# Kernel optimization log

Hardware: AMD Instinct MI355X
Metric: run time of the kernel (lower is better)

## Reference

```python
import jax, jax.numpy as jnp
import numpy as np

N_NODES = 100000
EMB_DIM = 64
HIDDEN = 8
OUT_DIM = 16
NUM_HEADS = 3
B = 1024
E_RAND = 3200000


def setup_inputs() -> dict:
    key = jax.random.key(0)
    ks = jax.random.split(key, 12)
    src = jax.random.randint(ks[0], (E_RAND,), 0, N_NODES, dtype=jnp.int32)
    dst = jax.random.randint(ks[1], (E_RAND,), 0, N_NODES, dtype=jnp.int32)
    loop = jnp.arange(N_NODES, dtype=jnp.int32)
    src = jnp.concatenate([src, loop])
    dst = jnp.concatenate([dst, loop])
    # multi-hot query indicator, ~50 items per query, guarantee >=1 item
    queries = (jax.random.uniform(ks[2], (B, N_NODES)) < 5e-4).astype(jnp.float32)
    queries = queries.at[:, 0].set(1.0)
    pos_items = jax.random.randint(ks[3], (B,), 0, N_NODES, dtype=jnp.int32)
    neg_items = jax.random.randint(ks[4], (B,), 0, N_NODES, dtype=jnp.int32)
    embedding = jax.random.normal(ks[5], (N_NODES, EMB_DIM), dtype=jnp.float32) * 0.1
    # GAT layer 1: NUM_HEADS heads, in=64 -> out=8 per head (concat)
    W1 = jax.random.normal(ks[6], (NUM_HEADS, EMB_DIM, HIDDEN), dtype=jnp.float32) * 0.1
    a1 = jax.random.normal(ks[7], (NUM_HEADS, 2 * HIDDEN), dtype=jnp.float32) * 0.1
    # GAT layer 2: 1 head, in=24 -> out=16
    W2 = jax.random.normal(ks[8], (NUM_HEADS * HIDDEN, OUT_DIM), dtype=jnp.float32) * 0.1
    a2 = jax.random.normal(ks[9], (2 * OUT_DIM,), dtype=jnp.float32) * 0.1
    return {"queries": queries, "pos_items": pos_items, "neg_items": neg_items,
            "embedding": embedding, "W1": W1, "a1": a1, "W2": W2, "a2": a2,
            "src": src, "dst": dst}


def gat_layer(h, W, a, src, dst, n_nodes):
    # h: [N, in], W: [H, in, o], a: [H, 2o]; returns [N, H, o]
    o = W.shape[-1]
    z = jnp.einsum('nd,hdo->nho', h, W)            # [N,H,o]
    zs, zd = z[src], z[dst]                         # [E,H,o]
    e = jax.nn.leaky_relu(
        jnp.einsum('eho,ho->eh', zs, a[:, :o]) +
        jnp.einsum('eho,ho->eh', zd, a[:, o:]), 0.01)  # [E,H]
    m = jax.ops.segment_max(e, dst, num_segments=n_nodes)       # [N,H]
    alpha = jnp.exp(e - m[dst])                                  # [E,H]
    denom = jax.ops.segment_sum(alpha, dst, num_segments=n_nodes)
    num = jax.ops.segment_sum(alpha[:, :, None] * zs, dst, num_segments=n_nodes)
    return num / denom[:, :, None]


def gat_forward(embedding, W1, a1, W2, a2, src, dst):
    n = embedding.shape[0]
    h1 = gat_layer(embedding, W1, a1, src, dst, n)       # [N,H,hid]
    h1 = jax.nn.elu(h1.reshape(n, -1))                   # [N,H*hid]
    h2 = gat_layer(h1, W2[None], a2[None], src, dst, n)  # [N,1,out]
    return h2[:, 0]                                      # [N,out]


def reference(queries, pos_items, neg_items, embedding, W1, a1, W2, a2, src, dst):
    item_embeds = gat_forward(embedding, W1, a1, W2, a2, src, dst)  # [N,16]
    item_cnt = jnp.sum(queries, axis=1)                              # [B]
    query_embeds = jnp.matmul(queries, item_embeds) / item_cnt[:, None]
    pos_embed = item_embeds[pos_items]
    neg_embed = item_embeds[neg_items]
    return (query_embeds, pos_embed, neg_embed)
```

## Files before the change

kernel.cpp:

```cpp
#include <hip/hip_runtime.h>

#define NH 3
#define HID 8
#define C1 24
#define C2 16
#define BSH 5
#define BNODES 32
#define NBMAX 3200
#define SCAP 1792
#define PCHUNK 16384
#define AZS 32

__global__ __launch_bounds__(256) void k_z1(
    const float* __restrict__ emb, const float* __restrict__ W1g,
    const float* __restrict__ a1g, float* __restrict__ az1,
    float4* __restrict__ f1d, int N) {
    __shared__ float sW[NH * 64 * HID];
    __shared__ float sa[NH * 2 * HID];
    for (int i = threadIdx.x; i < NH * 64 * HID; i += blockDim.x) sW[i] = W1g[i];
    for (int i = threadIdx.x; i < NH * 2 * HID; i += blockDim.x) sa[i] = a1g[i];
    __syncthreads();
    int n = blockIdx.x * blockDim.x + threadIdx.x;
    if (n >= N) return;
    float e[64];
    const float4* ep = (const float4*)(emb + (size_t)n * 64);
#pragma unroll
    for (int i = 0; i < 16; ++i) {
        float4 v = ep[i];
        e[4*i+0] = v.x; e[4*i+1] = v.y; e[4*i+2] = v.z; e[4*i+3] = v.w;
    }
    float z[C1];
#pragma unroll
    for (int c = 0; c < C1; ++c) z[c] = 0.f;
    for (int d = 0; d < 64; ++d) {
        float ed = e[d];
#pragma unroll
        for (int h = 0; h < NH; ++h) {
            const float4* wp = (const float4*)&sW[(h * 64 + d) * HID];
            float4 w0 = wp[0], w1 = wp[1];
            z[h*HID+0] += ed * w0.x; z[h*HID+1] += ed * w0.y;
            z[h*HID+2] += ed * w0.z; z[h*HID+3] += ed * w0.w;
            z[h*HID+4] += ed * w1.x; z[h*HID+5] += ed * w1.y;
            z[h*HID+6] += ed * w1.z; z[h*HID+7] += ed * w1.w;
        }
    }
    float fs[NH], fd[NH];
#pragma unroll
    for (int h = 0; h < NH; ++h) {
        float s = 0.f, dsum = 0.f;
#pragma unroll
        for (int o = 0; o < HID; ++o) {
            s    += z[h*HID+o] * sa[h*2*HID + o];
            dsum += z[h*HID+o] * sa[h*2*HID + HID + o];
        }
        fs[h] = s; fd[h] = dsum;
    }
    float4* zp = (float4*)(az1 + (size_t)n * AZS);
    zp[0] = make_float4(fs[0], fs[1], fs[2], 0.f);
#pragma unroll
    for (int i = 0; i < 6; ++i)
        zp[1 + i] = make_float4(z[4*i], z[4*i+1], z[4*i+2], z[4*i+3]);
    zp[7] = make_float4(0.f, 0.f, 0.f, 0.f);
    f1d[n] = make_float4(fd[0], fd[1], fd[2], 0.f);
}

__global__ void k_zero(int* __restrict__ p, int n) {
    int i = blockIdx.x * blockDim.x + threadIdx.x;
    if (i < n) p[i] = 0;
}

__global__ __launch_bounds__(256) void k_count(const int* __restrict__ dst,
                                               int* __restrict__ bcnt, int E, int NB) {
    __shared__ int lh[NBMAX];
    for (int i = threadIdx.x; i < NB; i += 256) lh[i] = 0;
    __syncthreads();
    int base = blockIdx.x * PCHUNK;
    int end = base + PCHUNK; if (end > E) end = E;
    for (int i = base + threadIdx.x; i < end; i += 256)
        atomicAdd(&lh[dst[i] >> BSH], 1);
    __syncthreads();
    for (int i = threadIdx.x; i < NB; i += 256)
        if (lh[i]) atomicAdd(&bcnt[i], lh[i]);
}

#define SCANK 13
__global__ __launch_bounds__(256) void k_bscan(const int* __restrict__ bcnt,
                                               int* __restrict__ boff,
                                               int* __restrict__ bcur,
                                               int* __restrict__ rowptr,
                                               int NB, int N, int E) {
    __shared__ int sd[256];
    int tid = threadIdx.x;
    int v[SCANK]; int tsum = 0;
#pragma unroll
    for (int i = 0; i < SCANK; ++i) {
        int g = tid * SCANK + i;
        v[i] = (g < NB) ? bcnt[g] : 0;
        tsum += v[i];
    }
    sd[tid] = tsum; __syncthreads();
    for (int off = 1; off < 256; off <<= 1) {
        int t = (tid >= off) ? sd[tid - off] : 0;
        __syncthreads();
        sd[tid] += t;
        __syncthreads();
    }
    int pref = sd[tid] - tsum;
#pragma unroll
    for (int i = 0; i < SCANK; ++i) {
        int g = tid * SCANK + i;
        if (g < NB) { boff[g] = pref; bcur[g] = pref; pref += v[i]; }
    }
    if (tid == 255) boff[NB] = pref;
    if (tid == 0) rowptr[N] = E;
}

__global__ __launch_bounds__(256) void k_part(const int* __restrict__ src,
                                              const int* __restrict__ dst,
                                              int* __restrict__ bcur,
                                              int* __restrict__ bedges, int E, int NB) {
    __shared__ int lh[NBMAX];
    __shared__ int lbase[NBMAX];
    for (int i = threadIdx.x; i < NB; i += 256) lh[i] = 0;
    __syncthreads();
    int base = blockIdx.x * PCHUNK;
    int end = base + PCHUNK; if (end > E) end = E;
    for (int i = base + threadIdx.x; i < end; i += 256)
        atomicAdd(&lh[dst[i] >> BSH], 1);
    __syncthreads();
    for (int i = threadIdx.x; i < NB; i += 256) {
        int c = lh[i];
        lbase[i] = c ? atomicAdd(&bcur[i], c) : 0;
        lh[i] = 0;
    }
    __syncthreads();
    for (int i = base + threadIdx.x; i < end; i += 256) {
        int d = dst[i];
        int b = d >> BSH;
        int p = lbase[b] + atomicAdd(&lh[b], 1);
        bedges[p] = src[i] | ((d & (BNODES - 1)) << 17);
    }
}

__global__ __launch_bounds__(256) void k_gat1(
    const int* __restrict__ boff, int* __restrict__ bedges,
    const float* __restrict__ az1, const float4* __restrict__ f1d,
    const float* __restrict__ W2g, const float* __restrict__ a2g,
    float* __restrict__ z2, float* __restrict__ f2s, float* __restrict__ f2d,
    int* __restrict__ rowptr, int N) {
    __shared__ int ssrc[SCAP];
    __shared__ int scnt[BNODES];
    __shared__ int sstart[BNODES + 1];
    __shared__ int scur[BNODES];
    __shared__ float sW2[C1 * C2];
    __shared__ float sa2[2 * C2];
    int tid = threadIdx.x;
    int b = blockIdx.x;
    int beg = boff[b], cnt = boff[b + 1] - beg;
    if (tid < BNODES) scnt[tid] = 0;
    for (int i = tid; i < C1 * C2; i += 256) sW2[i] = W2g[i];
    if (tid < 2 * C2) sa2[tid] = a2g[tid];
    __syncthreads();
    for (int i = tid; i < cnt; i += 256)
        atomicAdd(&scnt[bedges[beg + i] >> 17], 1);
    __syncthreads();
    if (tid < BNODES) {
        int v = scnt[tid];
        int x = v;
        for (int d = 1; d < BNODES; d <<= 1) {
            int t = __shfl_up(x, d, 64);
            if (tid >= d) x += t;
        }
        sstart[tid] = x - v;
        scur[tid] = x - v;
        if (tid == BNODES - 1) sstart[BNODES] = x;
    }
    __syncthreads();
    for (int i = tid; i < cnt; i += 256) {
        int pk = bedges[beg + i];
        int p = atomicAdd(&scur[pk >> 17], 1);
        ssrc[p] = pk & 0x1FFFF;
    }
    __syncthreads();
    for (int i = tid; i < cnt; i += 256) bedges[beg + i] = ssrc[i];
    int n0 = b << BSH;
    if (tid < BNODES) rowptr[n0 + tid] = beg + sstart[tid];
    int nl = tid >> 3, l8 = tid & 7;
    int n = n0 + nl;
    int s0 = sstart[nl], s1 = sstart[nl + 1];
    float4 fdv = (n < N) ? f1d[n] : make_float4(0.f, 0.f, 0.f, 0.f);
    float acc[C1];
#pragma unroll
    for (int c = 0; c < C1; ++c) acc[c] = 0.f;
    float den0 = 0.f, den1 = 0.f, den2 = 0.f;
    for (int i = s0 + l8; i < s1; i += 8) {
        int s = ssrc[i];
        const float4* zp = (const float4*)(az1 + ((size_t)s << 5));
        float4 q0 = zp[0], q1 = zp[1], q2 = zp[2], q3 = zp[3],
               q4 = zp[4], q5 = zp[5], q6 = zp[6];
        float e0 = q0.x + fdv.x, e1 = q0.y + fdv.y, e2 = q0.z + fdv.z;
        e0 = e0 > 0.f ? e0 : 0.01f * e0;
        e1 = e1 > 0.f ? e1 : 0.01f * e1;
        e2 = e2 > 0.f ? e2 : 0.01f * e2;
        float a0 = __expf(e0), a1 = __expf(e1), a2v = __expf(e2);
        den0 += a0; den1 += a1; den2 += a2v;
        acc[0]  += a0 * q1.x; acc[1]  += a0 * q1.y; acc[2]  += a0 * q1.z; acc[3]  += a0 * q1.w;
        acc[4]  += a0 * q2.x; acc[5]  += a0 * q2.y; acc[6]  += a0 * q2.z; acc[7]  += a0 * q2.w;
        acc[8]  += a1 * q3.x; acc[9]  += a1 * q3.y; acc[10] += a1 * q3.z; acc[11] += a1 * q3.w;
        acc[12] += a1 * q4.x; acc[13] += a1 * q4.y; acc[14] += a1 * q4.z; acc[15] += a1 * q4.w;
        acc[16] += a2v * q5.x; acc[17] += a2v * q5.y; acc[18] += a2v * q5.z; acc[19] += a2v * q5.w;
        acc[20] += a2v * q6.x; acc[21] += a2v * q6.y; acc[22] += a2v * q6.z; acc[23] += a2v * q6.w;
    }
#pragma unroll
    for (int c = 0; c < C1; ++c) {
        acc[c] += __shfl_xor(acc[c], 1, 64);
        acc[c] += __shfl_xor(acc[c], 2, 64);
        acc[c] += __shfl_xor(acc[c], 4, 64);
    }
    den0 += __shfl_xor(den0, 1, 64); den0 += __shfl_xor(den0, 2, 64); den0 += __shfl_xor(den0, 4, 64);
    den1 += __shfl_xor(den1, 1, 64); den1 += __shfl_xor(den1, 2, 64); den1 += __shfl_xor(den1, 4, 64);
    den2 += __shfl_xor(den2, 1, 64); den2 += __shfl_xor(den2, 2, 64); den2 += __shfl_xor(den2, 4, 64);
    if (l8 == 0 && n < N) {
        float h1v[C1];
        float inv0 = 1.f / den0, inv1 = 1.f / den1, inv2 = 1.f / den2;
#pragma unroll
        for (int o = 0; o < HID; ++o) {
            float v0 = acc[o] * inv0;
            float v1 = acc[HID + o] * inv1;
            float v2 = acc[2 * HID + o] * inv2;
            h1v[o]           = v0 > 0.f ? v0 : (__expf(v0) - 1.f);
            h1v[HID + o]     = v1 > 0.f ? v1 : (__expf(v1) - 1.f);
            h1v[2 * HID + o] = v2 > 0.f ? v2 : (__expf(v2) - 1.f);
        }
        float zz[C2];
#pragma unroll
        for (int k = 0; k < C2; ++k) zz[k] = 0.f;
        for (int c = 0; c < C1; ++c) {
            float hv = h1v[c];
#pragma unroll
            for (int k = 0; k < C2; ++k) zz[k] += hv * sW2[c * C2 + k];
        }
        float fs = 0.f, fdd = 0.f;
#pragma unroll
        for (int k = 0; k < C2; ++k) {
            fs  += zz[k] * sa2[k];
            fdd += zz[k] * sa2[C2 + k];
        }
        float4* zo = (float4*)(z2 + (size_t)n * C2);
#pragma unroll
        for (int i = 0; i < 4; ++i)
            zo[i] = make_float4(zz[4*i], zz[4*i+1], zz[4*i+2], zz[4*i+3]);
        f2s[n] = fs;
        f2d[n] = fdd;
    }
}

__global__ __launch_bounds__(256) void k_gat2(
    const int* __restrict__ rowptr, const int* __restrict__ csr,
    const float* __restrict__ z2, const float* __restrict__ f2s,
    const float* __restrict__ f2d, float* __restrict__ item, int N) {
    int t = blockIdx.x * blockDim.x + threadIdx.x;
    int n = t >> 3, l8 = t & 7;
    if (n >= N) return;
    int beg = rowptr[n], end = rowptr[n + 1];
    float fdv = f2d[n];
    float acc[C2];
#pragma unroll
    for (int k = 0; k < C2; ++k) acc[k] = 0.f;
    float den = 0.f;
    for (int i = beg + l8; i < end; i += 8) {
        int s = csr[i];
        float e = f2s[s] + fdv;
        e = e > 0.f ? e : 0.01f * e;
        float a = __expf(e);
        den += a;
        const float4* zp = (const float4*)(z2 + (size_t)s * C2);
        float4 q0 = zp[0], q1 = zp[1], q2 = zp[2], q3 = zp[3];
        acc[0]  += a * q0.x; acc[1]  += a * q0.y; acc[2]  += a * q0.z; acc[3]  += a * q0.w;
        acc[4]  += a * q1.x; acc[5]  += a * q1.y; acc[6]  += a * q1.z; acc[7]  += a * q1.w;
        acc[8]  += a * q2.x; acc[9]  += a * q2.y; acc[10] += a * q2.z; acc[11] += a * q2.w;
        acc[12] += a * q3.x; acc[13] += a * q3.y; acc[14] += a * q3.z; acc[15] += a * q3.w;
    }
#pragma unroll
    for (int k = 0; k < C2; ++k) {
        acc[k] += __shfl_xor(acc[k], 1, 64);
        acc[k] += __shfl_xor(acc[k], 2, 64);
        acc[k] += __shfl_xor(acc[k], 4, 64);
    }
    den += __shfl_xor(den, 1, 64);
    den += __shfl_xor(den, 2, 64);
    den += __shfl_xor(den, 4, 64);
    if (l8 == 0) {
        float inv = 1.f / den;
        float4* io = (float4*)(item + (size_t)n * C2);
#pragma unroll
        for (int i = 0; i < 4; ++i)
            io[i] = make_float4(acc[4*i]*inv, acc[4*i+1]*inv, acc[4*i+2]*inv, acc[4*i+3]*inv);
    }
}

__global__ __launch_bounds__(256) void k_query(
    const float* __restrict__ queries, const float* __restrict__ item,
    float* __restrict__ out, int N) {
    int b = blockIdx.x;
    const float4* qrow = (const float4*)(queries + (size_t)b * N);
    int n4 = N >> 2;
    float acc[C2];
#pragma unroll
    for (int k = 0; k < C2; ++k) acc[k] = 0.f;
    float cnt = 0.f;
    for (int i = threadIdx.x; i < n4; i += 256) {
        float4 v = qrow[i];
        int j = i * 4;
        float vv[4] = {v.x, v.y, v.z, v.w};
#pragma unroll
        for (int c = 0; c < 4; ++c) {
            if (vv[c] != 0.f) {
                cnt += vv[c];
                const float4* rp = (const float4*)(item + (size_t)(j + c) * C2);
                float4 r0 = rp[0], r1 = rp[1], r2 = rp[2], r3 = rp[3];
                acc[0]  += vv[c]*r0.x; acc[1]  += vv[c]*r0.y; acc[2]  += vv[c]*r0.z; acc[3]  += vv[c]*r0.w;
                acc[4]  += vv[c]*r1.x; acc[5]  += vv[c]*r1.y; acc[6]  += vv[c]*r1.z; acc[7]  += vv[c]*r1.w;
                acc[8]  += vv[c]*r2.x; acc[9]  += vv[c]*r2.y; acc[10] += vv[c]*r2.z; acc[11] += vv[c]*r2.w;
                acc[12] += vv[c]*r3.x; acc[13] += vv[c]*r3.y; acc[14] += vv[c]*r3.z; acc[15] += vv[c]*r3.w;
            }
        }
    }
    int rem = N & 3;
    if ((int)threadIdx.x < rem) {
        int j = n4 * 4 + threadIdx.x;
        float qv = queries[(size_t)b * N + j];
        if (qv != 0.f) {
            cnt += qv;
#pragma unroll
            for (int k = 0; k < C2; ++k) acc[k] += qv * item[(size_t)j * C2 + k];
        }
    }
    __shared__ float red[4][C2 + 1];
    int lane = threadIdx.x & 63, wid = threadIdx.x >> 6;
#pragma unroll
    for (int k = 0; k < C2; ++k)
        for (int off = 32; off; off >>= 1) acc[k] += __shfl_down(acc[k], off, 64);
    for (int off = 32; off; off >>= 1) cnt += __shfl_down(cnt, off, 64);
    if (lane == 0) {
#pragma unroll
        for (int k = 0; k < C2; ++k) red[wid][k] = acc[k];
        red[wid][C2] = cnt;
    }
    __syncthreads();
    if (threadIdx.x < C2 + 1) {
        float s = red[0][threadIdx.x] + red[1][threadIdx.x] +
                  red[2][threadIdx.x] + red[3][threadIdx.x];
        red[0][threadIdx.x] = s;
    }
    __syncthreads();
    if (threadIdx.x < C2)
        out[(size_t)b * C2 + threadIdx.x] = red[0][threadIdx.x] / red[0][C2];
}

__global__ void k_posneg(const int* __restrict__ pos, const int* __restrict__ neg,
                         const float* __restrict__ item, float* __restrict__ out, int B) {
    int idx = blockIdx.x * blockDim.x + threadIdx.x;
    int total = 2 * B * C2;
    if (idx >= total) return;
    int which = idx / (B * C2);
    int r = idx - which * B * C2;
    int b = r / C2, k = r - b * C2;
    int node = which ? neg[b] : pos[b];
    out[(size_t)B * C2 + idx] = item[(size_t)node * C2 + k];
}

extern "C" void kernel_launch(void* const* d_in, const int* in_sizes, int n_in,
                              void* d_out, int out_size, void* d_ws, size_t ws_size,
                              hipStream_t stream) {
    const float* queries = (const float*)d_in[0];
    const int*   pos     = (const int*)d_in[1];
    const int*   neg     = (const int*)d_in[2];
    const float* emb     = (const float*)d_in[3];
    const float* W1      = (const float*)d_in[4];
    const float* a1      = (const float*)d_in[5];
    const float* W2      = (const float*)d_in[6];
    const float* a2      = (const float*)d_in[7];
    const int*   src     = (const int*)d_in[8];
    const int*   dst     = (const int*)d_in[9];

    int B = in_sizes[1];
    int N = in_sizes[3] / 64;
    int E = in_sizes[8];
    float* out = (float*)d_out;

    int NB = (N + BNODES - 1) >> BSH;

    char* w = (char*)d_ws;
    auto alloc = [&](size_t bytes) -> char* {
        char* p = w;
        w += (bytes + 255) & ~(size_t)255;
        return p;
    };
    float*  az1    = (float*)alloc(sizeof(float) * (size_t)N * AZS);
    float4* f1d    = (float4*)alloc(sizeof(float4) * (size_t)N);
    float*  z2     = (float*)alloc(sizeof(float) * (size_t)N * C2);
    float*  f2s    = (float*)alloc(sizeof(float) * (size_t)N);
    float*  f2d    = (float*)alloc(sizeof(float) * (size_t)N);
    float*  item   = (float*)alloc(sizeof(float) * (size_t)N * C2);
    int*    bcnt   = (int*)alloc(sizeof(int) * (size_t)NB);
    int*    boff   = (int*)alloc(sizeof(int) * (size_t)(NB + 1));
    int*    bcur   = (int*)alloc(sizeof(int) * (size_t)NB);
    int*    rowptr = (int*)alloc(sizeof(int) * (size_t)(N + 1));
    int*    bedges = (int*)alloc(sizeof(int) * (size_t)E);

    int nblkN = (N + 255) / 256;
    int nPart = (E + PCHUNK - 1) / PCHUNK;

    k_z1<<<nblkN, 256, 0, stream>>>(emb, W1, a1, az1, f1d, N);
    k_zero<<<(NB + 255) / 256, 256, 0, stream>>>(bcnt, NB);
    k_count<<<nPart, 256, 0, stream>>>(dst, bcnt, E, NB);
    k_bscan<<<1, 256, 0, stream>>>(bcnt, boff, bcur, rowptr, NB, N, E);
    k_part<<<nPart, 256, 0, stream>>>(src, dst, bcur, bedges, E, NB);
    k_gat1<<<NB, 256, 0, stream>>>(boff, bedges, az1, f1d, W2, a2,
                                   z2, f2s, f2d, rowptr, N);
    k_gat2<<<(N * 8 + 255) / 256, 256, 0, stream>>>(rowptr, bedges, z2, f2s, f2d, item, N);
    k_query<<<B, 256, 0, stream>>>(queries, item, out, N);
    k_posneg<<<(2 * B * C2 + 255) / 256, 256, 0, stream>>>(pos, neg, item, out, B);
}
```

Baseline: 857.0 us.

## Store gathered node features in fp16 and fold small kernels together

Measured after the change: 893.5 us. 4.3% more time.

```diff
diff --git a/kernel.cpp b/kernel.cpp
--- a/kernel.cpp
+++ b/kernel.cpp
@@ -1,4 +1,5 @@
 #include <hip/hip_runtime.h>
+#include <hip/hip_fp16.h>
 
 #define NH 3
 #define HID 8
@@ -8,19 +9,26 @@
 #define BNODES 32
 #define NBMAX 3200
 #define SCAP 1792
-#define PCHUNK 16384
+#define PCHUNK 32768
 #define AZS 32
+
+__device__ inline float2 cvt2(unsigned u) {
+    __half2 h;
+    *reinterpret_cast<unsigned*>(&h) = u;
+    return __half22float2(h);
+}
 
 __global__ __launch_bounds__(256) void k_z1(
     const float* __restrict__ emb, const float* __restrict__ W1g,
-    const float* __restrict__ a1g, float* __restrict__ az1,
-    float4* __restrict__ f1d, int N) {
+    const float* __restrict__ a1g, __half* __restrict__ az1h,
+    float4* __restrict__ f1d, int* __restrict__ bcnt, int NB, int N) {
     __shared__ float sW[NH * 64 * HID];
     __shared__ float sa[NH * 2 * HID];
     for (int i = threadIdx.x; i < NH * 64 * HID; i += blockDim.x) sW[i] = W1g[i];
     for (int i = threadIdx.x; i < NH * 2 * HID; i += blockDim.x) sa[i] = a1g[i];
-    __syncthreads();
     int n = blockIdx.x * blockDim.x + threadIdx.x;
+    if (n < NB) bcnt[n] = 0;
+    __syncthreads();
     if (n >= N) return;
     float e[64];
     const float4* ep = (const float4*)(emb + (size_t)n * 64);
@@ -55,18 +63,17 @@
         }
         fs[h] = s; fd[h] = dsum;
     }
-    float4* zp = (float4*)(az1 + (size_t)n * AZS);
-    zp[0] = make_float4(fs[0], fs[1], fs[2], 0.f);
-#pragma unroll
-    for (int i = 0; i < 6; ++i)
-        zp[1 + i] = make_float4(z[4*i], z[4*i+1], z[4*i+2], z[4*i+3]);
-    zp[7] = make_float4(0.f, 0.f, 0.f, 0.f);
+    __half hb[32];
+    hb[0] = __float2half_rn(fs[0]); hb[1] = __float2half_rn(fs[1]);
+    hb[2] = __float2half_rn(fs[2]); hb[3] = __half(0.f);
+#pragma unroll
+    for (int o = 0; o < C1; ++o) hb[4 + o] = __float2half_rn(z[o]);
+#pragma unroll
+    for (int o = 28; o < 32; ++o) hb[o] = __half(0.f);
+    uint4* zo = (uint4*)(az1h + ((size_t)n << 5));
+    const uint4* hbu = (const uint4*)hb;
+    zo[0] = hbu[0]; zo[1] = hbu[1]; zo[2] = hbu[2]; zo[3] = hbu[3];
     f1d[n] = make_float4(fd[0], fd[1], fd[2], 0.f);
-}
-
-__global__ void k_zero(int* __restrict__ p, int n) {
-    int i = blockIdx.x * blockDim.x + threadIdx.x;
-    if (i < n) p[i] = 0;
 }
 
 __global__ __launch_bounds__(256) void k_count(const int* __restrict__ dst,
@@ -144,9 +151,9 @@
 
 __global__ __launch_bounds__(256) void k_gat1(
     const int* __restrict__ boff, int* __restrict__ bedges,
-    const float* __restrict__ az1, const float4* __restrict__ f1d,
+    const __half* __restrict__ az1h, const float4* __restrict__ f1d,
     const float* __restrict__ W2g, const float* __restrict__ a2g,
-    float* __restrict__ z2, float* __restrict__ f2s, float* __restrict__ f2d,
+    __half* __restrict__ z2h, float* __restrict__ f2s, float* __restrict__ f2d,
     int* __restrict__ rowptr, int N) {
     __shared__ int ssrc[SCAP];
     __shared__ int scnt[BNODES];
@@ -195,21 +202,31 @@
     float den0 = 0.f, den1 = 0.f, den2 = 0.f;
     for (int i = s0 + l8; i < s1; i += 8) {
         int s = ssrc[i];
-        const float4* zp = (const float4*)(az1 + ((size_t)s << 5));
-        float4 q0 = zp[0], q1 = zp[1], q2 = zp[2], q3 = zp[3],
-               q4 = zp[4], q5 = zp[5], q6 = zp[6];
-        float e0 = q0.x + fdv.x, e1 = q0.y + fdv.y, e2 = q0.z + fdv.z;
+        const uint4* up = (const uint4*)(az1h + ((size_t)s << 5));
+        uint4 u0 = up[0], u1 = up[1], u2 = up[2], u3 = up[3];
+        float2 p01 = cvt2(u0.x), p2x = cvt2(u0.y);
+        float e0 = p01.x + fdv.x, e1 = p01.y + fdv.y, e2 = p2x.x + fdv.z;
         e0 = e0 > 0.f ? e0 : 0.01f * e0;
         e1 = e1 > 0.f ? e1 : 0.01f * e1;
         e2 = e2 > 0.f ? e2 : 0.01f * e2;
         float a0 = __expf(e0), a1 = __expf(e1), a2v = __expf(e2);
         den0 += a0; den1 += a1; den2 += a2v;
-        acc[0]  += a0 * q1.x; acc[1]  += a0 * q1.y; acc[2]  += a0 * q1.z; acc[3]  += a0 * q1.w;
-        acc[4]  += a0 * q2.x; acc[5]  += a0 * q2.y; acc[6]  += a0 * q2.z; acc[7]  += a0 * q2.w;
-        acc[8]  += a1 * q3.x; acc[9]  += a1 * q3.y; acc[10] += a1 * q3.z; acc[11] += a1 * q3.w;
-        acc[12] += a1 * q4.x; acc[13] += a1 * q4.y; acc[14] += a1 * q4.z; acc[15] += a1 * q4.w;
-        acc[16] += a2v * q5.x; acc[17] += a2v * q5.y; acc[18] += a2v * q5.z; acc[19] += a2v * q5.w;
-        acc[20] += a2v * q6.x; acc[21] += a2v * q6.y; acc[22] += a2v * q6.z; acc[23] += a2v * q6.w;
+        float2 z0 = cvt2(u0.z), z1 = cvt2(u0.w);
+        float2 z2v = cvt2(u1.x), z3 = cvt2(u1.y), z4 = cvt2(u1.z), z5 = cvt2(u1.w);
+        float2 z6 = cvt2(u2.x), z7 = cvt2(u2.y), z8 = cvt2(u2.z), z9 = cvt2(u2.w);
+        float2 z10 = cvt2(u3.x), z11 = cvt2(u3.y);
+        acc[0]  += a0 * z0.x;  acc[1]  += a0 * z0.y;
+        acc[2]  += a0 * z1.x;  acc[3]  += a0 * z1.y;
+        acc[4]  += a0 * z2v.x; acc[5]  += a0 * z2v.y;
+        acc[6]  += a0 * z3.x;  acc[7]  += a0 * z3.y;
+        acc[8]  += a1 * z4.x;  acc[9]  += a1 * z4.y;
+        acc[10] += a1 * z5.x;  acc[11] += a1 * z5.y;
+        acc[12] += a1 * z6.x;  acc[13] += a1 * z6.y;
+        acc[14] += a1 * z7.x;  acc[15] += a1 * z7.y;
+        acc[16] += a2v * z8.x;  acc[17] += a2v * z8.y;
+        acc[18] += a2v * z9.x;  acc[19] += a2v * z9.y;
+        acc[20] += a2v * z10.x; acc[21] += a2v * z10.y;
+        acc[22] += a2v * z11.x; acc[23] += a2v * z11.y;
     }
 #pragma unroll
     for (int c = 0; c < C1; ++c) {
@@ -246,10 +263,12 @@
             fs  += zz[k] * sa2[k];
             fdd += zz[k] * sa2[C2 + k];
         }
-        float4* zo = (float4*)(z2 + (size_t)n * C2);
-#pragma unroll
-        for (int i = 0; i < 4; ++i)
-            zo[i] = make_float4(zz[4*i], zz[4*i+1], zz[4*i+2], zz[4*i+3]);
+        __half zb[16];
+#pragma unroll
+        for (int k = 0; k < C2; ++k) zb[k] = __float2half_rn(zz[k]);
+        uint4* zo = (uint4*)(z2h + ((size_t)n << 4));
+        const uint4* zbu = (const uint4*)zb;
+        zo[0] = zbu[0]; zo[1] = zbu[1];
         f2s[n] = fs;
         f2d[n] = fdd;
     }
@@ -257,7 +276,7 @@
 
 __global__ __launch_bounds__(256) void k_gat2(
     const int* __restrict__ rowptr, const int* __restrict__ csr,
-    const float* __restrict__ z2, const float* __restrict__ f2s,
+    const __half* __restrict__ z2h, const float* __restrict__ f2s,
     const float* __restrict__ f2d, float* __restrict__ item, int N) {
     int t = blockIdx.x * blockDim.x + threadIdx.x;
     int n = t >> 3, l8 = t & 7;
@@ -274,12 +293,18 @@
         e = e > 0.f ? e : 0.01f * e;
         float a = __expf(e);
         den += a;
-        const float4* zp = (const float4*)(z2 + (size_t)s * C2);
-        float4 q0 = zp[0], q1 = zp[1], q2 = zp[2], q3 = zp[3];
-        acc[0]  += a * q0.x; acc[1]  += a * q0.y; acc[2]  += a * q0.z; acc[3]  += a * q0.w;
-        acc[4]  += a * q1.x; acc[5]  += a * q1.y; acc[6]  += a * q1.z; acc[7]  += a * q1.w;
-        acc[8]  += a * q2.x; acc[9]  += a * q2.y; acc[10] += a * q2.z; acc[11] += a * q2.w;
-        acc[12] += a * q3.x; acc[13] += a * q3.y; acc[14] += a * q3.z; acc[15] += a * q3.w;
+        const uint4* zp = (const uint4*)(z2h + ((size_t)s << 4));
+        uint4 u0 = zp[0], u1 = zp[1];
+        float2 z0 = cvt2(u0.x), z1 = cvt2(u0.y), z2v = cvt2(u0.z), z3 = cvt2(u0.w);
+        float2 z4 = cvt2(u1.x), z5 = cvt2(u1.y), z6 = cvt2(u1.z), z7 = cvt2(u1.w);
+        acc[0]  += a * z0.x;  acc[1]  += a * z0.y;
+        acc[2]  += a * z1.x;  acc[3]  += a * z1.y;
+        acc[4]  += a * z2v.x; acc[5]  += a * z2v.y;
+        acc[6]  += a * z3.x;  acc[7]  += a * z3.y;
+        acc[8]  += a * z4.x;  acc[9]  += a * z4.y;
+        acc[10] += a * z5.x;  acc[11] += a * z5.y;
+        acc[12] += a * z6.x;  acc[13] += a * z6.y;
+        acc[14] += a * z7.x;  acc[15] += a * z7.y;
     }
 #pragma unroll
     for (int k = 0; k < C2; ++k) {
@@ -301,7 +326,8 @@
 
 __global__ __launch_bounds__(256) void k_query(
     const float* __restrict__ queries, const float* __restrict__ item,
-    float* __restrict__ out, int N) {
+    const int* __restrict__ pos, const int* __restrict__ neg,
+    float* __restrict__ out, int N, int B) {
     int b = blockIdx.x;
     const float4* qrow = (const float4*)(queries + (size_t)b * N);
     int n4 = N >> 2;
@@ -356,18 +382,12 @@
     __syncthreads();
     if (threadIdx.x < C2)
         out[(size_t)b * C2 + threadIdx.x] = red[0][threadIdx.x] / red[0][C2];
-}
-
-__global__ void k_posneg(const int* __restrict__ pos, const int* __restrict__ neg,
-                         const float* __restrict__ item, float* __restrict__ out, int B) {
-    int idx = blockIdx.x * blockDim.x + threadIdx.x;
-    int total = 2 * B * C2;
-    if (idx >= total) return;
-    int which = idx / (B * C2);
-    int r = idx - which * B * C2;
-    int b = r / C2, k = r - b * C2;
-    int node = which ? neg[b] : pos[b];
-    out[(size_t)B * C2 + idx] = item[(size_t)node * C2 + k];
+    else if (threadIdx.x >= 64 && threadIdx.x < 64 + C2)
+        out[((size_t)B + b) * C2 + (threadIdx.x - 64)] =
+            item[(size_t)pos[b] * C2 + (threadIdx.x - 64)];
+    else if (threadIdx.x >= 128 && threadIdx.x < 128 + C2)
+        out[((size_t)2 * B + b) * C2 + (threadIdx.x - 128)] =
+            item[(size_t)neg[b] * C2 + (threadIdx.x - 128)];
 }
 
 extern "C" void kernel_launch(void* const* d_in, const int* in_sizes, int n_in,
@@ -397,9 +417,9 @@
         w += (bytes + 255) & ~(size_t)255;
         return p;
     };
-    float*  az1    = (float*)alloc(sizeof(float) * (size_t)N * AZS);
+    __half* az1h   = (__half*)alloc(sizeof(__half) * (size_t)N * AZS);
     float4* f1d    = (float4*)alloc(sizeof(float4) * (size_t)N);
-    float*  z2     = (float*)alloc(sizeof(float) * (size_t)N * C2);
+    __half* z2h    = (__half*)alloc(sizeof(__half) * (size_t)N * C2);
     float*  f2s    = (float*)alloc(sizeof(float) * (size_t)N);
     float*  f2d    = (float*)alloc(sizeof(float) * (size_t)N);
     float*  item   = (float*)alloc(sizeof(float) * (size_t)N * C2);
@@ -412,14 +432,12 @@
     int nblkN = (N + 255) / 256;
     int nPart = (E + PCHUNK - 1) / PCHUNK;
 
-    k_z1<<<nblkN, 256, 0, stream>>>(emb, W1, a1, az1, f1d, N);
-    k_zero<<<(NB + 255) / 256, 256, 0, stream>>>(bcnt, NB);
+    k_z1<<<nblkN, 256, 0, stream>>>(emb, W1, a1, az1h, f1d, bcnt, NB, N);
     k_count<<<nPart, 256, 0, stream>>>(dst, bcnt, E, NB);
     k_bscan<<<1, 256, 0, stream>>>(bcnt, boff, bcur, rowptr, NB, N, E);
     k_part<<<nPart, 256, 0, stream>>>(src, dst, bcur, bedges, E, NB);
-    k_gat1<<<NB, 256, 0, stream>>>(boff, bedges, az1, f1d, W2, a2,
-                                   z2, f2s, f2d, rowptr, N);
-    k_gat2<<<(N * 8 + 255) / 256, 256, 0, stream>>>(rowptr, bedges, z2, f2s, f2d, item, N);
-    k_query<<<B, 256, 0, stream>>>(queries, item, out, N);
-    k_posneg<<<(2 * B * C2 + 255) / 256, 256, 0, stream>>>(pos, neg, item, out, B);
-}
+    k_gat1<<<NB, 256, 0, stream>>>(boff, bedges, az1h, f1d, W2, a2,
+                                   z2h, f2s, f2d, rowptr, N);
+    k_gat2<<<(N * 8 + 255) / 256, 256, 0, stream>>>(rowptr, bedges, z2h, f2s, f2d, item, N);
+    k_query<<<B, 256, 0, stream>>>(queries, item, pos, neg, out, N, B);
+}
```
